# Kernel optimization log

Hardware: AMD Instinct MI355X
Metric: run time of the kernel (lower is better)

The kernel has to match this reference:

```python
import jax, jax.numpy as jnp
import numpy as np
from jax import lax

B, H, N, F = 32, 168, 512, 8
P_STEPS = 24


def setup_inputs() -> dict:
    key = jax.random.key(0)
    ks = jax.random.split(key, 8)
    s = 0.02
    return {
        "x": jax.random.normal(ks[0], (B, H, N, F), dtype=jnp.float32),
        "conv_w": jax.random.normal(ks[1], (N * F, N), dtype=jnp.float32) * s,
        "conv_b": jnp.zeros((N,), dtype=jnp.float32),
        "lstm_k": jax.random.normal(ks[2], (N, 4 * N), dtype=jnp.float32) * s,
        "lstm_rk": jax.random.normal(ks[3], (N, 4 * N), dtype=jnp.float32) * s,
        "lstm_b": jnp.zeros((4 * N,), dtype=jnp.float32),
        "dense_w": jax.random.normal(ks[4], (N, N), dtype=jnp.float32) * s,
        "dense_b": jnp.zeros((N,), dtype=jnp.float32),
        "P": P_STEPS,
    }


def _lstm_cell(h, c, x_t, lstm_k, lstm_rk, lstm_b):
    # Keras LSTMCell gate order: i, f, g(candidate), o
    z = x_t @ lstm_k + h @ lstm_rk + lstm_b  # [B, 4N]
    i, f, g, o = jnp.split(z, 4, axis=-1)
    i = jax.nn.sigmoid(i)
    f = jax.nn.sigmoid(f)
    g = jnp.tanh(g)
    o = jax.nn.sigmoid(o)
    c_new = f * c + i * g
    h_new = o * jnp.tanh(c_new)
    return h_new, c_new


def reference(x, conv_w, conv_b, lstm_k, lstm_rk, lstm_b, dense_w, dense_b, P):
    b, hh, n, f = x.shape
    # Conv1D kernel_size=1 == per-timestep dense projection N*F -> N
    xr = x.reshape(b, hh, n * f) @ conv_w + conv_b  # [B, H, N]

    h0 = jnp.zeros((b, n), dtype=x.dtype)
    c0 = jnp.zeros((b, n), dtype=x.dtype)

    def enc_step(carry, x_t):
        h, c = carry
        h, c = _lstm_cell(h, c, x_t, lstm_k, lstm_rk, lstm_b)
        return (h, c), None

    (h, c), _ = lax.scan(enc_step, (h0, c0), xr.transpose(1, 0, 2))

    def dec_step(carry, _):
        h, c = carry
        h2, c2 = _lstm_cell(h, c, h, lstm_k, lstm_rk, lstm_b)
        return (h2, c2), h2

    _, preds = lax.scan(dec_step, (h, c), None, length=P)  # [P, B, N]
    preds = preds.transpose(1, 0, 2)  # [B, P, N]
    return preds @ dense_w + dense_b
```

## Files before the change

### kernel.cpp

```cpp
#include <hip/hip_runtime.h>
#include <hip/hip_bf16.h>
#include <math.h>

typedef __hip_bfloat16 bf16;
typedef __attribute__((ext_vector_type(8))) short short8;
typedef __attribute__((ext_vector_type(4))) float floatx4;

#define B_  32
#define H_  168
#define N_  512
#define P_  24
#define NF_ 4096
#define G4N 2048
#define M1  (B_*H_)
#define NX  (M1*NF_)
#define TSTEPS (H_+P_)
#define NWG 64
#define HSZ (B_*N_)

#define NB_CVT  (NX / 4 / 256)
#define NB_CWT  ((N_/32) * (NF_/32))
#define NB_K3   ((G4N/32) * (N_/32))
#define NB_DWT  ((N_/32) * (N_/32))
#define NB_PREP (NB_CVT + NB_CWT + NB_K3 + NB_DWT + 1)

__global__ __launch_bounds__(256) void prep_all(
    const float* __restrict__ x,
    const float* __restrict__ conv_w,
    const float* __restrict__ lstm_k,
    const float* __restrict__ lstm_rk,
    const float* __restrict__ dense_w,
    bf16* __restrict__ xb,
    bf16* __restrict__ cwT,
    bf16* __restrict__ kT,
    bf16* __restrict__ rkT,
    bf16* __restrict__ wcT,
    bf16* __restrict__ dwT,
    bf16* __restrict__ hring,
    unsigned* __restrict__ bar) {
  __shared__ float t1[32][33];
  __shared__ float t2[32][33];
  int bid = blockIdx.x, tid = threadIdx.x;

  if (bid < NB_CVT) {
    int i = bid * 256 + tid;
    float4 v = ((const float4*)x)[i];
    bf16 o[4] = {__float2bfloat16(v.x), __float2bfloat16(v.y),
                 __float2bfloat16(v.z), __float2bfloat16(v.w)};
    *(ulong1*)(xb + (size_t)i * 4) = *(ulong1*)o;
    return;
  }
  int tx = tid & 31, ty = tid >> 5;

  if (bid < NB_CVT + NB_CWT) {
    int local = bid - NB_CVT;
    int bx = local & 15, by = local >> 4;
    const int R = NF_, C = N_;
#pragma unroll
    for (int yy = 0; yy < 32; yy += 8)
      t1[ty + yy][tx] = conv_w[(size_t)(by * 32 + ty + yy) * C + bx * 32 + tx];
    __syncthreads();
#pragma unroll
    for (int yy = 0; yy < 32; yy += 8)
      cwT[(size_t)(bx * 32 + ty + yy) * R + by * 32 + tx] =
          __float2bfloat16(t1[tx][ty + yy]);
    return;
  }
  if (bid < NB_CVT + NB_CWT + NB_K3) {
    int local = bid - NB_CVT - NB_CWT;
    int bx = local & 63, by = local >> 6;
    const int R = N_, C = G4N;
#pragma unroll
    for (int yy = 0; yy < 32; yy += 8) {
      size_t idx = (size_t)(by * 32 + ty + yy) * C + bx * 32 + tx;
      t1[ty + yy][tx] = lstm_k[idx];
      t2[ty + yy][tx] = lstm_rk[idx];
    }
    __syncthreads();
#pragma unroll
    for (int yy = 0; yy < 32; yy += 8) {
      size_t o = (size_t)(bx * 32 + ty + yy) * R + by * 32 + tx;
      float kv = t1[tx][ty + yy], rv = t2[tx][ty + yy];
      kT[o]  = __float2bfloat16(kv);
      rkT[o] = __float2bfloat16(rv);
      wcT[o] = __float2bfloat16(kv + rv);
    }
    return;
  }
  if (bid < NB_CVT + NB_CWT + NB_K3 + NB_DWT) {
    int local = bid - NB_CVT - NB_CWT - NB_K3;
    int bx = local & 15, by = local >> 4;
    const int R = N_, C = N_;
#pragma unroll
    for (int yy = 0; yy < 32; yy += 8)
      t1[ty + yy][tx] = dense_w[(size_t)(by * 32 + ty + yy) * C + bx * 32 + tx];
    __syncthreads();
#pragma unroll
    for (int yy = 0; yy < 32; yy += 8)
      dwT[(size_t)(bx * 32 + ty + yy) * R + by * 32 + tx] =
          __float2bfloat16(t1[tx][ty + yy]);
    return;
  }
  unsigned long long* hz = (unsigned long long*)hring;
#pragma unroll
  for (int k = 0; k < 16; ++k) hz[k * 256 + tid] = 0ull;
  if (tid < TSTEPS) bar[tid] = 0u;
}

template <bool OUT_BF16>
__global__ __launch_bounds__(256) void gemm_bt(const bf16* __restrict__ A,
                                               const bf16* __restrict__ BT,
                                               const float* __restrict__ bias,
                                               void* __restrict__ Cout,
                                               int M, int N, int K, int permute) {
  __shared__ short As[128 * 40];
  __shared__ short Bs[128 * 40];
  int tid  = threadIdx.x;
  int wave = tid >> 6, lane = tid & 63;
  int wm = wave >> 1, wn = wave & 1;
  int quad = lane >> 4, l16 = lane & 15;
  int m0 = blockIdx.y * 128, n0 = blockIdx.x * 128;

  floatx4 acc[4][4];
#pragma unroll
  for (int i = 0; i < 4; i++)
#pragma unroll
    for (int j = 0; j < 4; j++) acc[i][j] = (floatx4){0.f, 0.f, 0.f, 0.f};

  int r0 = tid >> 2;
  int c0 = (tid & 3) * 8;

  for (int k0 = 0; k0 < K; k0 += 32) {
    short8 a0 = *(const short8*)(A  + (size_t)(m0 + r0)      * K + k0 + c0);
    short8 a1 = *(const short8*)(A  + (size_t)(m0 + r0 + 64) * K + k0 + c0);
    short8 b0 = *(const short8*)(BT + (size_t)(n0 + r0)      * K + k0 + c0);
    short8 b1 = *(const short8*)(BT + (size_t)(n0 + r0 + 64) * K + k0 + c0);
    __syncthreads();
    *(short8*)(&As[r0 * 40 + c0])        = a0;
    *(short8*)(&As[(r0 + 64) * 40 + c0]) = a1;
    *(short8*)(&Bs[r0 * 40 + c0])        = b0;
    *(short8*)(&Bs[(r0 + 64) * 40 + c0]) = b1;
    __syncthreads();
    short8 af[4], bfr[4];
#pragma unroll
    for (int i = 0; i < 4; i++)
      af[i] = *(const short8*)(&As[(wm * 64 + i * 16 + l16) * 40 + quad * 8]);
#pragma unroll
    for (int j = 0; j < 4; j++)
      bfr[j] = *(const short8*)(&Bs[(wn * 64 + j * 16 + l16) * 40 + quad * 8]);
#pragma unroll
    for (int i = 0; i < 4; i++)
#pragma unroll
      for (int j = 0; j < 4; j++)
        acc[i][j] = __builtin_amdgcn_mfma_f32_16x16x32_bf16(af[i], bfr[j],
                                                            acc[i][j], 0, 0, 0);
  }
#pragma unroll
  for (int i = 0; i < 4; i++) {
    int row = m0 + wm * 64 + i * 16 + quad * 4;
#pragma unroll
    for (int j = 0; j < 4; j++) {
      int col = n0 + wn * 64 + j * 16 + l16;
      float bv = bias ? bias[col] : 0.f;
#pragma unroll
      for (int r = 0; r < 4; r++) {
        int gr = row + r;
        int orow = permute ? (gr % H_) * B_ + gr / H_ : gr;
        float v = acc[i][j][r] + bv;
        if (OUT_BF16)
          ((bf16*)Cout)[(size_t)orow * N + col] = __float2bfloat16(v);
        else
          ((float*)Cout)[(size_t)orow * N + col] = v;
      }
    }
  }
}

__global__ __launch_bounds__(256) void lstm_persist(
    const bf16* __restrict__ rkT,
    const bf16* __restrict__ wcT,
    const float* __restrict__ bvec,
    const float* __restrict__ xk,
    bf16* __restrict__ hring,
    bf16* __restrict__ preds,
    unsigned* __restrict__ bar) {
  __shared__ short Wenc[32][520];
  __shared__ short Wdec[32][520];
  __shared__ float zs[32][33];
  __shared__ bf16  hstage[32][8];

  int tid  = threadIdx.x;
  int wave = tid >> 6, lane = tid & 63;
  int tm = wave >> 1, tn = wave & 1;
  int quad = lane >> 4, l16 = lane & 15;
  int n0 = blockIdx.x * 8;
  int lc   = tn * 16 + l16;
  int gcol = ((lc >> 3) << 9) + n0 + (lc & 7);
  int brow = tm * 16 + quad * 4;

  for (int idx = tid; idx < 32 * 64; idx += 256) {
    int r = idx >> 6, ck = (idx & 63) << 3;
    int grow = ((r >> 3) << 9) + n0 + (r & 7);
    *(short8*)&Wenc[r][ck] = *(const short8*)(rkT + (size_t)grow * 512 + ck);
    *(short8*)&Wdec[r][ck] = *(const short8*)(wcT + (size_t)grow * 512 + ck);
  }
  float bias_r = bvec[gcol];
  int b = tid >> 3, j = tid & 7;
  int nn = n0 + j;
  float c_reg = 0.f;

  float xkv[4];
  {
    const float* xp = xk + (size_t)brow * G4N + gcol;
#pragma unroll
    for (int r = 0; r < 4; ++r) xkv[r] = xp[(size_t)r * G4N];
  }
  __syncthreads();

  for (int t = 0; t < TSTEPS; ++t) {
    const bf16* h_in  = hring + (size_t)t * HSZ;
    bf16*       h_out = hring + (size_t)(t + 1) * HSZ;
    const short(*Ws)[520] = (t < H_) ? Wenc : Wdec;

    float xn[4] = {0.f, 0.f, 0.f, 0.f};
    if (t + 1 < H_) {
      const float* xp = xk + (size_t)((t + 1) * B_ + brow) * G4N + gcol;
#pragma unroll
      for (int r = 0; r < 4; ++r) xn[r] = xp[(size_t)r * G4N];
    }

    floatx4 acc0 = (floatx4){0.f, 0.f, 0.f, 0.f};
    floatx4 acc1 = (floatx4){0.f, 0.f, 0.f, 0.f};
    const bf16*  ap = h_in + (size_t)(tm * 16 + l16) * 512 + quad * 8;
    const short* bp = &Ws[lc][quad * 8];
#pragma unroll
    for (int k0 = 0; k0 < 512; k0 += 64) {
      short8 av0 = *(const short8*)(ap + k0);
      short8 av1 = *(const short8*)(ap + k0 + 32);
      short8 bv0 = *(const short8*)(bp + k0);
      short8 bv1 = *(const short8*)(bp + k0 + 32);
      acc0 = __builtin_amdgcn_mfma_f32_16x16x32_bf16(av0, bv0, acc0, 0, 0, 0);
      acc1 = __builtin_amdgcn_mfma_f32_16x16x32_bf16(av1, bv1, acc1, 0, 0, 0);
    }
    floatx4 acc = acc0 + acc1;
#pragma unroll
    for (int r = 0; r < 4; ++r)
      zs[brow + r][lc] = acc[r] + bias_r + xkv[r];
    __syncthreads();

    float zi = zs[b][j], zf = zs[b][8 + j], zg = zs[b][16 + j], zo = zs[b][24 + j];
    float ig = 1.f / (1.f + __expf(-zi));
    float fg = 1.f / (1.f + __expf(-zf));
    float gg = tanhf(zg);
    float og = 1.f / (1.f + __expf(-zo));
    c_reg = fg * c_reg + ig * gg;
    float hn = og * tanhf(c_reg);
    hstage[b][j] = __float2bfloat16(hn);
    if (t >= H_)
      preds[(size_t)b * (P_ * N_) + (t - H_) * N_ + nn] = __float2bfloat16(hn);
    __syncthreads();

    if (tid < 64) {
      int bb = tid >> 1, f4 = (tid & 1) * 4;
      unsigned long long v = *(const unsigned long long*)&hstage[bb][f4];
      __hip_atomic_store((unsigned long long*)(h_out + bb * 512 + n0 + f4), v,
                         __ATOMIC_RELAXED, __HIP_MEMORY_SCOPE_AGENT);
    }
    __syncthreads();

    if (t + 1 < TSTEPS) {
      if (tid == 0) {
        unsigned old = __hip_atomic_fetch_add(&bar[t], 1u, __ATOMIC_RELAXED,
                                              __HIP_MEMORY_SCOPE_AGENT);
        if (old != NWG - 1) {
          while (__hip_atomic_load(&bar[t], __ATOMIC_RELAXED,
                                   __HIP_MEMORY_SCOPE_AGENT) < NWG)
            __builtin_amdgcn_s_sleep(1);
        }
      }
      __builtin_amdgcn_fence(__ATOMIC_ACQUIRE, "workgroup");
      __syncthreads();
    }
#pragma unroll
    for (int r = 0; r < 4; ++r) xkv[r] = xn[r];
  }
}

extern "C" void kernel_launch(void* const* d_in, const int* in_sizes, int n_in,
                              void* d_out, int out_size, void* d_ws, size_t ws_size,
                              hipStream_t stream) {
  const float* x       = (const float*)d_in[0];
  const float* conv_w  = (const float*)d_in[1];
  const float* conv_b  = (const float*)d_in[2];
  const float* lstm_k  = (const float*)d_in[3];
  const float* lstm_rk = (const float*)d_in[4];
  const float* lstm_b  = (const float*)d_in[5];
  const float* dense_w = (const float*)d_in[6];
  const float* dense_b = (const float*)d_in[7];
  float* out = (float*)d_out;

  char* p = (char*)d_ws;
  auto carve = [&](size_t bytes) {
    char* r = p;
    p += (bytes + 255) & ~(size_t)255;
    return r;
  };
  bf16*  xb    = (bf16*)carve((size_t)NX * 2);
  bf16*  xr    = (bf16*)carve((size_t)M1 * N_ * 2);
  float* xk    = (float*)carve((size_t)M1 * G4N * 4);
  bf16*  cwT   = (bf16*)carve((size_t)N_ * NF_ * 2);
  bf16*  kT    = (bf16*)carve((size_t)G4N * N_ * 2);
  bf16*  rkT   = (bf16*)carve((size_t)G4N * N_ * 2);
  bf16*  wcT   = (bf16*)carve((size_t)G4N * N_ * 2);
  bf16*  dwT   = (bf16*)carve((size_t)N_ * N_ * 2);
  bf16*  preds = (bf16*)carve((size_t)B_ * P_ * N_ * 2);
  bf16*  hring = (bf16*)carve((size_t)(TSTEPS + 1) * HSZ * 2);
  unsigned* bar  = (unsigned*)carve((size_t)TSTEPS * 4);

  prep_all<<<NB_PREP, 256, 0, stream>>>(x, conv_w, lstm_k, lstm_rk, dense_w,
                                        xb, cwT, kT, rkT, wcT, dwT, hring, bar);

  gemm_bt<true><<<dim3(N_ / 128, M1 / 128), 256, 0, stream>>>(xb, cwT, conv_b, xr,
                                                              M1, N_, NF_, 1);
  gemm_bt<false><<<dim3(G4N / 128, M1 / 128), 256, 0, stream>>>(xr, kT, nullptr,
                                                                xk, M1, G4N, N_, 0);

  lstm_persist<<<NWG, 256, 0, stream>>>(rkT, wcT, lstm_b, xk, hring, preds, bar);

  gemm_bt<false><<<dim3(N_ / 128, (B_ * P_) / 128), 256, 0, stream>>>(
      preds, dwT, dense_b, out, B_ * P_, N_, N_, 0);
}
```

Baseline: 1.025 ms.

## Fuse dense output GEMM into persistent LSTM kernel and prefetch GEMM tiles

The final dense projection GEMM is folded into the tail of the persistent LSTM kernel. After the last timestep all workgroups pass a grid barrier, and the first 24 blocks compute the output tiles from preds, which are now written with agent-scope atomic stores so other blocks can see them. This removes one kernel launch and its launch gap. The shared GEMM tile routine also register-prefetches the next K slice while the current one is computed. In exchange the LSTM kernel uses more LDS and adds one extra barrier step.

```diff
diff --git a/kernel.cpp b/kernel.cpp
--- a/kernel.cpp
+++ b/kernel.cpp
@@ -108,18 +108,16 @@
 }
 
 template <bool OUT_BF16>
-__global__ __launch_bounds__(256) void gemm_bt(const bf16* __restrict__ A,
-                                               const bf16* __restrict__ BT,
-                                               const float* __restrict__ bias,
-                                               void* __restrict__ Cout,
-                                               int M, int N, int K, int permute) {
-  __shared__ short As[128 * 40];
-  __shared__ short Bs[128 * 40];
+__device__ __forceinline__ void gemm_tile(
+    const bf16* __restrict__ A, const bf16* __restrict__ BT,
+    const float* __restrict__ bias, void* __restrict__ Cout,
+    int M, int N, int K, int permute, int bx, int by,
+    short* __restrict__ As, short* __restrict__ Bs) {
   int tid  = threadIdx.x;
   int wave = tid >> 6, lane = tid & 63;
   int wm = wave >> 1, wn = wave & 1;
   int quad = lane >> 4, l16 = lane & 15;
-  int m0 = blockIdx.y * 128, n0 = blockIdx.x * 128;
+  int m0 = by * 128, n0 = bx * 128;
 
   floatx4 acc[4][4];
 #pragma unroll
@@ -129,18 +127,28 @@
 
   int r0 = tid >> 2;
   int c0 = (tid & 3) * 8;
+  const bf16* pa0 = A  + (size_t)(m0 + r0)      * K + c0;
+  const bf16* pa1 = A  + (size_t)(m0 + r0 + 64) * K + c0;
+  const bf16* pb0 = BT + (size_t)(n0 + r0)      * K + c0;
+  const bf16* pb1 = BT + (size_t)(n0 + r0 + 64) * K + c0;
+  short8 a0 = *(const short8*)pa0;
+  short8 a1 = *(const short8*)pa1;
+  short8 b0 = *(const short8*)pb0;
+  short8 b1 = *(const short8*)pb1;
 
   for (int k0 = 0; k0 < K; k0 += 32) {
-    short8 a0 = *(const short8*)(A  + (size_t)(m0 + r0)      * K + k0 + c0);
-    short8 a1 = *(const short8*)(A  + (size_t)(m0 + r0 + 64) * K + k0 + c0);
-    short8 b0 = *(const short8*)(BT + (size_t)(n0 + r0)      * K + k0 + c0);
-    short8 b1 = *(const short8*)(BT + (size_t)(n0 + r0 + 64) * K + k0 + c0);
     __syncthreads();
     *(short8*)(&As[r0 * 40 + c0])        = a0;
     *(short8*)(&As[(r0 + 64) * 40 + c0]) = a1;
     *(short8*)(&Bs[r0 * 40 + c0])        = b0;
     *(short8*)(&Bs[(r0 + 64) * 40 + c0]) = b1;
     __syncthreads();
+    if (k0 + 32 < K) {
+      a0 = *(const short8*)(pa0 + k0 + 32);
+      a1 = *(const short8*)(pa1 + k0 + 32);
+      b0 = *(const short8*)(pb0 + k0 + 32);
+      b1 = *(const short8*)(pb1 + k0 + 32);
+    }
     short8 af[4], bfr[4];
 #pragma unroll
     for (int i = 0; i < 4; i++)
@@ -176,6 +184,18 @@
   }
 }
 
+template <bool OUT_BF16>
+__global__ __launch_bounds__(256) void gemm_bt(const bf16* __restrict__ A,
+                                               const bf16* __restrict__ BT,
+                                               const float* __restrict__ bias,
+                                               void* __restrict__ Cout,
+                                               int M, int N, int K, int permute) {
+  __shared__ short As[128 * 40];
+  __shared__ short Bs[128 * 40];
+  gemm_tile<OUT_BF16>(A, BT, bias, Cout, M, N, K, permute,
+                      blockIdx.x, blockIdx.y, As, Bs);
+}
+
 __global__ __launch_bounds__(256) void lstm_persist(
     const bf16* __restrict__ rkT,
     const bf16* __restrict__ wcT,
@@ -183,11 +203,16 @@
     const float* __restrict__ xk,
     bf16* __restrict__ hring,
     bf16* __restrict__ preds,
-    unsigned* __restrict__ bar) {
+    unsigned* __restrict__ bar,
+    const bf16* __restrict__ dwT,
+    const float* __restrict__ dbias,
+    float* __restrict__ out) {
   __shared__ short Wenc[32][520];
   __shared__ short Wdec[32][520];
   __shared__ float zs[32][33];
   __shared__ bf16  hstage[32][8];
+  __shared__ short As[128 * 40];
+  __shared__ short Bs[128 * 40];
 
   int tid  = threadIdx.x;
   int wave = tid >> 6, lane = tid & 63;
@@ -255,9 +280,13 @@
     float og = 1.f / (1.f + __expf(-zo));
     c_reg = fg * c_reg + ig * gg;
     float hn = og * tanhf(c_reg);
-    hstage[b][j] = __float2bfloat16(hn);
-    if (t >= H_)
-      preds[(size_t)b * (P_ * N_) + (t - H_) * N_ + nn] = __float2bfloat16(hn);
+    bf16 hv = __float2bfloat16(hn);
+    hstage[b][j] = hv;
+    if (t >= H_) {
+      __hip_atomic_store(
+          (unsigned short*)preds + (size_t)b * (P_ * N_) + (t - H_) * N_ + nn,
+          *(unsigned short*)&hv, __ATOMIC_RELAXED, __HIP_MEMORY_SCOPE_AGENT);
+    }
     __syncthreads();
 
     if (tid < 64) {
@@ -268,21 +297,25 @@
     }
     __syncthreads();
 
-    if (t + 1 < TSTEPS) {
-      if (tid == 0) {
-        unsigned old = __hip_atomic_fetch_add(&bar[t], 1u, __ATOMIC_RELAXED,
-                                              __HIP_MEMORY_SCOPE_AGENT);
-        if (old != NWG - 1) {
-          while (__hip_atomic_load(&bar[t], __ATOMIC_RELAXED,
-                                   __HIP_MEMORY_SCOPE_AGENT) < NWG)
-            __builtin_amdgcn_s_sleep(1);
-        }
+    if (tid == 0) {
+      unsigned old = __hip_atomic_fetch_add(&bar[t], 1u, __ATOMIC_RELAXED,
+                                            __HIP_MEMORY_SCOPE_AGENT);
+      if (old != NWG - 1) {
+        while (__hip_atomic_load(&bar[t], __ATOMIC_RELAXED,
+                                 __HIP_MEMORY_SCOPE_AGENT) < NWG)
+          __builtin_amdgcn_s_sleep(1);
       }
-      __builtin_amdgcn_fence(__ATOMIC_ACQUIRE, "workgroup");
-      __syncthreads();
-    }
+    }
+    __builtin_amdgcn_fence(__ATOMIC_ACQUIRE, "workgroup");
+    __syncthreads();
 #pragma unroll
     for (int r = 0; r < 4; ++r) xkv[r] = xn[r];
+  }
+
+  if (blockIdx.x < (B_ * P_ / 128) * (N_ / 128)) {
+    int bx = blockIdx.x & 3, by = blockIdx.x >> 2;
+    gemm_tile<false>(preds, dwT, dbias, out, B_ * P_, N_, N_, 0, bx, by,
+                     &As[0], &Bs[0]);
   }
 }
 
@@ -325,8 +358,6 @@
   gemm_bt<false><<<dim3(G4N / 128, M1 / 128), 256, 0, stream>>>(xr, kT, nullptr,
                                                                 xk, M1, G4N, N_, 0);
 
-  lstm_persist<<<NWG, 256, 0, stream>>>(rkT, wcT, lstm_b, xk, hring, preds, bar);
-
-  gemm_bt<false><<<dim3(N_ / 128, (B_ * P_) / 128), 256, 0, stream>>>(
-      preds, dwT, dense_b, out, B_ * P_, N_, N_, 0);
-}
+  lstm_persist<<<NWG, 256, 0, stream>>>(rkT, wcT, lstm_b, xk, hring, preds, bar,
+                                        dwT, dense_b, out);
+}
```

Result: no change. 1.006 ms (-1.9%).
